# Kernel optimization log

Hardware: AMD Instinct MI355X
Metric: run time of the kernel (lower is better)

The kernel has to match this reference:

```python
import jax, jax.numpy as jnp
import numpy as np

EPS = 1e-5  # torch BatchNorm default eps, eval mode with running stats

def _bn(x, g, b, m, v):
    shp = (1, -1) + (1,) * (x.ndim - 2)
    return (x - m.reshape(shp)) * (g.reshape(shp) / jnp.sqrt(v.reshape(shp) + EPS)) + b.reshape(shp)

def _lrelu(x):
    return jnp.where(x > 0, x, 0.2 * x)

def setup_inputs() -> dict:
    key = jax.random.key(0)
    ks = jax.random.split(key, 20)
    B, N, K = 4, 2048, 32
    Cin, Cf, Co = 6, 64, 64  # in_channels, feat_channels, out_channels(==nhiddens)
    f32 = jnp.float32
    def randn(k, shape, s=1.0):
        return jax.random.normal(k, shape, f32) * s
    def bnp(k, c):
        k1, k2, k3, k4 = jax.random.split(k, 4)
        return (randn(k1, (c,)), randn(k2, (c,)), randn(k3, (c,), 0.1),
                jax.random.uniform(k4, (c,), f32, 0.5, 1.5))
    inp = {
        "x": randn(ks[0], (B, Cin, N, K)),          # knn_points
        "y": randn(ks[1], (B, Cf, N, K)),           # knn_feat
        "points": randn(ks[2], (B, Cin // 2, N)),
        "feat": randn(ks[3], (B, Cf // 2, N)),
        "Wq": randn(ks[4], (Cf, Cf // 2), 0.1),
        "Wpos1": randn(ks[5], (Cin, Cin // 2), 0.1),
        "Wpos2": randn(ks[6], (Cf, Cin), 0.1),
        "Wattn": randn(ks[7], (Co * Cin, Cf), 0.1),
        "Wlin": randn(ks[8], (Co, Co), 0.1),
        "Wres": randn(ks[9], (Co, Cf), 0.1),
    }
    for name, k, c in [("q", ks[10], Cf), ("p", ks[11], Cin), ("a", ks[12], Co * Cin),
                       ("1", ks[13], Co), ("l", ks[14], Co), ("r", ks[15], Co)]:
        g, b, m, v = bnp(k, c)
        inp["g" + name], inp["b" + name], inp["m" + name], inp["v" + name] = g, b, m, v
    return inp

def reference(x, y, points, feat, Wq, Wpos1, Wpos2, Wattn, Wlin, Wres,
              gq, bq, mq, vq, gp, bp, mp, vp, ga, ba, ma, va,
              g1, b1, m1, v1, gl, bl, ml, vl, gr, br, mr, vr):
    B, Cin, N, K = x.shape
    Cf = y.shape[1]
    Co = Wattn.shape[0] // Cin
    # query projection (conv1d 1x1 == per-point GEMM) + BN + LeakyReLU
    x_q = _lrelu(_bn(jnp.einsum('oi,bin->bon', Wq, feat), gq, bq, mq, vq))   # [B,Cf,N]
    # positional branch
    pos = _lrelu(_bn(jnp.einsum('oi,bin->bon', Wpos1, points), gp, bp, mp, vp))  # [B,Cin,N]
    pos = pos[:, :, :, None] - x                                             # [B,Cin,N,K]
    pos = jnp.einsum('oi,bink->bonk', Wpos2, pos)                            # [B,Cf,N,K]
    # vector (subtraction) attention, softmax over neighbors k
    attn = x_q[:, :, :, None] - y + pos                                      # [B,Cf,N,K]
    attn = jax.nn.softmax(attn / float(np.sqrt(Cf)), axis=-1)
    attn = _bn(jnp.einsum('oi,bink->bonk', Wattn, attn), ga, ba, ma, va)     # [B,Co*Cin,N,K]
    # per-point tiny matmul: [Co,Cin] @ [Cin] for every (b,n,k)
    attn = attn.transpose(0, 2, 3, 1).reshape(B, N, K, Co, Cin)
    out = jnp.einsum('bnkoi,bnki->bonk', attn, x.transpose(0, 2, 3, 1))      # [B,Co,N,K]
    h = _lrelu(_bn(out, g1, b1, m1, v1))
    h = _bn(jnp.einsum('oi,bink->bonk', Wlin, h), gl, bl, ml, vl)
    res = _bn(jnp.einsum('oi,bink->bonk', Wres, y), gr, br, mr, vr)
    return _lrelu(h + res)
```

## Files before the change

kernel.cpp:

```cpp
#include <hip/hip_runtime.h>

constexpr int NB  = 4;
constexpr int NPT = 2048;
constexpr int KNN = 32;
constexpr int CIN = 6;
constexpr int CF  = 64;
constexpr int CO  = 64;
constexpr float EPS = 1e-5f;

typedef short bf16x8 __attribute__((ext_vector_type(8)));
typedef float f32x4  __attribute__((ext_vector_type(4)));

constexpr size_t WS_WA  = 0;
constexpr size_t WS_WL  = 49152;
constexpr size_t WS_WR  = 57344;
constexpr size_t WS_BA  = 65536;
constexpr size_t WS_BNF = 67072;

__device__ __host__ inline unsigned short bf16_rne(float f) {
  unsigned u = __builtin_bit_cast(unsigned, f);
  u += 0x7fffu + ((u >> 16) & 1u);
  return (unsigned short)(u >> 16);
}

__global__ void setup_kernel(const float *Wattn, const float *Wlin, const float *Wres,
                             const float *ga, const float *ba, const float *ma, const float *va,
                             const float *g1, const float *b1, const float *m1, const float *v1,
                             const float *gl, const float *bl, const float *ml, const float *vl,
                             const float *gr, const float *br, const float *mr, const float *vr,
                             unsigned short *WAf, unsigned short *WLf, unsigned short *WRf,
                             float *baP, float *bnf) {
  const int t = blockIdx.x * blockDim.x + threadIdx.x;
  const int stride = gridDim.x * blockDim.x;
  for (int e = t; e < 6 * 4 * 2 * 64 * 8; e += stride) {
    const int j = e & 7, l = (e >> 3) & 63, ks = (e >> 9) & 1, ot = (e >> 10) & 3, i = e >> 12;
    const int m = l & 15, cg = l >> 4;
    const int cc = ks * 32 + cg * 8 + j;
    const int row = (ot * 16 + m) * CIN + i;
    const float sa = ga[row] * rsqrtf(va[row] + EPS);
    WAf[e] = bf16_rne(Wattn[row * CF + cc] * sa);
  }
  for (int e = t; e < 4 * 2 * 64 * 8; e += stride) {
    const int j = e & 7, l = (e >> 3) & 63, ks = (e >> 9) & 1, ot = e >> 10;
    const int m = l & 15;
    const int cc = ks * 32 + (l >> 4) * 8 + j;
    const int row = ot * 16 + m;
    const float sl = gl[row] * rsqrtf(vl[row] + EPS);
    const float sr = gr[row] * rsqrtf(vr[row] + EPS);
    WLf[e] = bf16_rne(Wlin[row * CF + cc] * sl);
    WRf[e] = bf16_rne(Wres[row * CF + cc] * sr);
  }
  for (int e = t; e < 384; e += stride) {
    const int i = e >> 6, o = e & 63;
    const int j0 = o * CIN + i;
    const float sa = ga[j0] * rsqrtf(va[j0] + EPS);
    baP[e] = ba[j0] - ma[j0] * sa;
  }
  for (int e = t; e < 64; e += stride) {
    const float s1v = g1[e] * rsqrtf(v1[e] + EPS);
    bnf[e]      = s1v;
    bnf[64 + e] = b1[e] - m1[e] * s1v;
    const float slv = gl[e] * rsqrtf(vl[e] + EPS);
    const float srv = gr[e] * rsqrtf(vr[e] + EPS);
    bnf[128 + e] = (bl[e] - ml[e] * slv) + (br[e] - mr[e] * srv);
  }
}

struct Params {
  const float *x, *y, *points, *feat;
  const float *Wq, *Wpos1, *Wpos2;
  const float *gq, *bq, *mq, *vq;
  const float *gp, *bp, *mp, *vp;
  const unsigned short *WAf, *WLf, *WRf;
  const float *baP, *bnf;
  float *out;
};

__global__ __launch_bounds__(256) void fused_pt_attn(Params p) {
  const int tid  = threadIdx.x;
  const int lane = tid & 63;
  const int wid  = tid >> 6;
  const int bid  = ((blockIdx.x & 7) << 8) + (blockIdx.x >> 3);
  const int pidx = bid * 4 + wid;
  const int b    = pidx >> 11;
  const int n    = pidx & (NPT - 1);

  __shared__ unsigned short s_B[4][2 * 2048];
  __shared__ float s_d[4][192];
  __shared__ float s_f[4][32];
  unsigned short *yB = s_B[wid];
  unsigned short *PB = s_B[wid] + 2048;
  float *dW = s_d[wid];
  float *fW = s_f[wid];

  float ftv = 0.f, ptv = 0.f;
  if (lane < 32) ftv = p.feat[((size_t)b * 32 + lane) * NPT + n];
  if (lane < 3)  ptv = p.points[((size_t)b * 3 + lane) * NPT + n];
  const int xi = lane >> 3, xk = (lane & 7) * 4;
  float4 x4 = make_float4(0.f, 0.f, 0.f, 0.f);
  if (lane < 48)
    x4 = *(const float4 *)(p.x + (((size_t)b * CIN + xi) * NPT + n) * KNN + xk);
  const float *w2p = p.Wpos2 + lane * 6;
  const float2 w2a = *(const float2 *)(w2p);
  const float2 w2b = *(const float2 *)(w2p + 2);
  const float2 w2c = *(const float2 *)(w2p + 4);
  const float w2[6] = {w2a.x, w2a.y, w2b.x, w2b.y, w2c.x, w2c.y};

  if (lane < 32) fW[lane] = ftv;

  const float pt0 = __shfl(ptv, 0), pt1 = __shfl(ptv, 1), pt2 = __shfl(ptv, 2);
  float pos1[6];
#pragma unroll
  for (int i = 0; i < 6; ++i) {
    const float a = p.Wpos1[i * 3 + 0] * pt0 + p.Wpos1[i * 3 + 1] * pt1 +
                    p.Wpos1[i * 3 + 2] * pt2;
    const float s = p.gp[i] * rsqrtf(p.vp[i] + EPS);
    const float v = fmaf(a, s, p.bp[i] - p.mp[i] * s);
    pos1[i] = v > 0.f ? v : 0.2f * v;
  }

  if (lane < 48) {
    float pi = pos1[0];
    pi = (xi == 1) ? pos1[1] : pi;
    pi = (xi == 2) ? pos1[2] : pi;
    pi = (xi == 3) ? pos1[3] : pi;
    pi = (xi == 4) ? pos1[4] : pi;
    pi = (xi == 5) ? pos1[5] : pi;
    *(float4 *)(dW + xi * 32 + xk) =
        make_float4(pi - x4.x, pi - x4.y, pi - x4.z, pi - x4.w);
  }

  float xq;
  {
    float acc = 0.f;
    const float *wq = p.Wq + lane * 32;
#pragma unroll
    for (int q = 0; q < 8; ++q) {
      const float4 w4 = *(const float4 *)(wq + q * 4);
      const float4 f4 = *(const float4 *)(fW + q * 4);
      acc = fmaf(w4.x, f4.x, fmaf(w4.y, f4.y, fmaf(w4.z, f4.z, fmaf(w4.w, f4.w, acc))));
    }
    const float s = p.gq[lane] * rsqrtf(p.vq[lane] + EPS);
    const float v = fmaf(acc, s, p.bq[lane] - p.mq[lane] * s);
    xq = v > 0.f ? v : 0.2f * v;
  }

  float pre[32];
#pragma unroll
  for (int k = 0; k < 32; ++k) pre[k] = 0.f;
#pragma unroll
  for (int i = 0; i < 6; ++i) {
    const float wv = w2[i];
#pragma unroll
    for (int q = 0; q < 8; ++q) {
      const float4 d4 = *(const float4 *)(dW + i * 32 + q * 4);
      pre[q * 4 + 0] = fmaf(wv, d4.x, pre[q * 4 + 0]);
      pre[q * 4 + 1] = fmaf(wv, d4.y, pre[q * 4 + 1]);
      pre[q * 4 + 2] = fmaf(wv, d4.z, pre[q * 4 + 2]);
      pre[q * 4 + 3] = fmaf(wv, d4.w, pre[q * 4 + 3]);
    }
  }

  const float *yrow = p.y + (((size_t)b * CF + lane) * NPT + n) * KNN;
#pragma unroll
  for (int q = 0; q < 8; ++q) {
    const float4 y4 = *(const float4 *)(yrow + q * 4);
    const float yv[4] = {y4.x, y4.y, y4.z, y4.w};
#pragma unroll
    for (int j = 0; j < 4; ++j) {
      const int k = q * 4 + j;
      yB[k * 64 + (lane ^ ((k & 7) << 3))] = bf16_rne(yv[j]);
      pre[k] = (xq - yv[j] + pre[k]) * 0.125f;
    }
  }

  float mx = pre[0];
#pragma unroll
  for (int k = 1; k < 32; ++k) mx = fmaxf(mx, pre[k]);
  float sum = 0.f;
#pragma unroll
  for (int k = 0; k < 32; ++k) { pre[k] = __expf(pre[k] - mx); sum += pre[k]; }
  const float inv = 1.f / sum;
#pragma unroll
  for (int k = 0; k < 32; ++k)
    PB[k * 64 + (lane ^ ((k & 7) << 3))] = bf16_rne(pre[k] * inv);

  const int og = lane >> 4, kl = lane & 15;

  float xvv[6][2];
#pragma unroll
  for (int i = 0; i < 6; ++i)
#pragma unroll
    for (int nt = 0; nt < 2; ++nt)
      xvv[i][nt] = pos1[i] - dW[i * 32 + kl + nt * 16];

  bf16x8 Ba[2][2];
#pragma unroll
  for (int ks = 0; ks < 2; ++ks)
#pragma unroll
    for (int nt = 0; nt < 2; ++nt) {
      const int kcol = kl + nt * 16;
      Ba[ks][nt] = *(const bf16x8 *)(PB + kcol * 64 + ((ks * 32 + og * 8) ^ ((kcol & 7) << 3)));
    }

  const bf16x8 *WAv = (const bf16x8 *)p.WAf;
#pragma unroll
  for (int ot = 0; ot < 4; ++ot) {
    float out1[2][4] = {{0.f, 0.f, 0.f, 0.f}, {0.f, 0.f, 0.f, 0.f}};
#pragma unroll
    for (int i = 0; i < 6; ++i) {
      const bf16x8 A0 = WAv[((i * 4 + ot) * 2 + 0) * 64 + lane];
      const bf16x8 A1 = WAv[((i * 4 + ot) * 2 + 1) * 64 + lane];
      const f32x4 ba4 = *(const f32x4 *)(p.baP + i * 64 + ot * 16 + og * 4);
#pragma unroll
      for (int nt = 0; nt < 2; ++nt) {
        f32x4 g = {0.f, 0.f, 0.f, 0.f};
        g = __builtin_amdgcn_mfma_f32_16x16x32_bf16(A0, Ba[0][nt], g, 0, 0, 0);
        g = __builtin_amdgcn_mfma_f32_16x16x32_bf16(A1, Ba[1][nt], g, 0, 0, 0);
        const float xv = xvv[i][nt];
#pragma unroll
        for (int r = 0; r < 4; ++r)
          out1[nt][r] = fmaf(g[r] + ba4[r], xv, out1[nt][r]);
      }
    }
    const f32x4 s14 = *(const f32x4 *)(p.bnf + 0 * 64 + ot * 16 + og * 4);
    const f32x4 b14 = *(const f32x4 *)(p.bnf + 1 * 64 + ot * 16 + og * 4);
#pragma unroll
    for (int nt = 0; nt < 2; ++nt) {
      const int kcol = kl + nt * 16;
      unsigned hp[4];
#pragma unroll
      for (int r = 0; r < 4; ++r) {
        const float t = fmaf(s14[r], out1[nt][r], b14[r]);
        hp[r] = bf16_rne(t > 0.f ? t : 0.2f * t);
      }
      const int idx = kcol * 64 + ((ot * 16 + og * 4) ^ ((kcol & 7) << 3));
      *(uint2 *)(PB + idx) = make_uint2(hp[0] | (hp[1] << 16), hp[2] | (hp[3] << 16));
    }
  }

  bf16x8 Bh[2][2], By[2][2];
#pragma unroll
  for (int ks = 0; ks < 2; ++ks)
#pragma unroll
    for (int nt = 0; nt < 2; ++nt) {
      const int kcol = kl + nt * 16;
      const int off = kcol * 64 + ((ks * 32 + og * 8) ^ ((kcol & 7) << 3));
      Bh[ks][nt] = *(const bf16x8 *)(PB + off);
      By[ks][nt] = *(const bf16x8 *)(yB + off);
    }
  const bf16x8 *WLv = (const bf16x8 *)p.WLf;
  const bf16x8 *WRv = (const bf16x8 *)p.WRf;
#pragma unroll
  for (int ot = 0; ot < 4; ++ot) {
    const bf16x8 L0 = WLv[(ot * 2 + 0) * 64 + lane];
    const bf16x8 L1 = WLv[(ot * 2 + 1) * 64 + lane];
    const bf16x8 R0 = WRv[(ot * 2 + 0) * 64 + lane];
    const bf16x8 R1 = WRv[(ot * 2 + 1) * 64 + lane];
    const f32x4 blr = *(const f32x4 *)(p.bnf + 2 * 64 + ot * 16 + og * 4);
#pragma unroll
    for (int nt = 0; nt < 2; ++nt) {
      f32x4 a = {0.f, 0.f, 0.f, 0.f};
      a = __builtin_amdgcn_mfma_f32_16x16x32_bf16(L0, Bh[0][nt], a, 0, 0, 0);
      a = __builtin_amdgcn_mfma_f32_16x16x32_bf16(L1, Bh[1][nt], a, 0, 0, 0);
      a = __builtin_amdgcn_mfma_f32_16x16x32_bf16(R0, By[0][nt], a, 0, 0, 0);
      a = __builtin_amdgcn_mfma_f32_16x16x32_bf16(R1, By[1][nt], a, 0, 0, 0);
      const int kcol = kl + nt * 16;
      float *ob = p.out + (((size_t)(b * CO + ot * 16 + og * 4)) * NPT + n) * KNN + kcol;
#pragma unroll
      for (int r = 0; r < 4; ++r) {
        const float v = a[r] + blr[r];
        ob[(size_t)r * NPT * KNN] = v > 0.f ? v : 0.2f * v;
      }
    }
  }
}

extern "C" void kernel_launch(void *const *d_in, const int *in_sizes, int n_in,
                              void *d_out, int out_size, void *d_ws, size_t ws_size,
                              hipStream_t stream) {
  char *ws = (char *)d_ws;
  unsigned short *WAf = (unsigned short *)(ws + WS_WA);
  unsigned short *WLf = (unsigned short *)(ws + WS_WL);
  unsigned short *WRf = (unsigned short *)(ws + WS_WR);
  float *baP = (float *)(ws + WS_BA);
  float *bnf = (float *)(ws + WS_BNF);

  setup_kernel<<<dim3(96), dim3(256), 0, stream>>>(
      (const float *)d_in[7], (const float *)d_in[8], (const float *)d_in[9],
      (const float *)d_in[18], (const float *)d_in[19], (const float *)d_in[20], (const float *)d_in[21],
      (const float *)d_in[22], (const float *)d_in[23], (const float *)d_in[24], (const float *)d_in[25],
      (const float *)d_in[26], (const float *)d_in[27], (const float *)d_in[28], (const float *)d_in[29],
      (const float *)d_in[30], (const float *)d_in[31], (const float *)d_in[32], (const float *)d_in[33],
      WAf, WLf, WRf, baP, bnf);

  Params p;
  p.x      = (const float *)d_in[0];
  p.y      = (const float *)d_in[1];
  p.points = (const float *)d_in[2];
  p.feat   = (const float *)d_in[3];
  p.Wq     = (const float *)d_in[4];
  p.Wpos1  = (const float *)d_in[5];
  p.Wpos2  = (const float *)d_in[6];
  p.gq = (const float *)d_in[10]; p.bq = (const float *)d_in[11];
  p.mq = (const float *)d_in[12]; p.vq = (const float *)d_in[13];
  p.gp = (const float *)d_in[14]; p.bp = (const float *)d_in[15];
  p.mp = (const float *)d_in[16]; p.vp = (const float *)d_in[17];
  p.WAf = WAf; p.WLf = WLf; p.WRf = WRf;
  p.baP = baP; p.bnf = bnf;
  p.out = (float *)d_out;

  fused_pt_attn<<<dim3(NB * NPT / 4), dim3(256), 0, stream>>>(p);
}
```

Before: 66.88 us.

## Split output-channel tiles across waves sharing point pairs to reuse weight fragments

Each wave used to process one point through all four output-channel tiles. Now pairs of waves share two points through shared memory, and each wave handles half the output tiles for both points. Each weight fragment loaded from global memory is therefore reused for two points, halving per-wave weight traffic. The positional-term algebra is also refactored so pos1·W2 folds into a per-lane scalar alpha. In exchange the kernel adds three block-wide barriers and keeps more live registers for two points' fragments.

After: 76.30 us. +14.1%, slower.

```diff
diff --git a/kernel.cpp b/kernel.cpp
--- a/kernel.cpp
+++ b/kernel.cpp
@@ -81,178 +81,203 @@
   const int lane = tid & 63;
   const int wid  = tid >> 6;
   const int bid  = ((blockIdx.x & 7) << 8) + (blockIdx.x >> 3);
-  const int pidx = bid * 4 + wid;
-  const int b    = pidx >> 11;
-  const int n    = pidx & (NPT - 1);
-
-  __shared__ unsigned short s_B[4][2 * 2048];
-  __shared__ float s_d[4][192];
+  const int b    = bid >> 9;
+  const int n    = (bid * 4 + wid) & (NPT - 1);
+
+  __shared__ unsigned short s_Y[4][2048];
+  __shared__ unsigned short s_P[4][2048];
+  __shared__ float s_x[4][192];
   __shared__ float s_f[4][32];
-  unsigned short *yB = s_B[wid];
-  unsigned short *PB = s_B[wid] + 2048;
-  float *dW = s_d[wid];
+  unsigned short *YB = s_Y[wid];
+  unsigned short *PB = s_P[wid];
+  float *xW = s_x[wid];
   float *fW = s_f[wid];
 
-  float ftv = 0.f, ptv = 0.f;
-  if (lane < 32) ftv = p.feat[((size_t)b * 32 + lane) * NPT + n];
-  if (lane < 3)  ptv = p.points[((size_t)b * 3 + lane) * NPT + n];
-  const int xi = lane >> 3, xk = (lane & 7) * 4;
-  float4 x4 = make_float4(0.f, 0.f, 0.f, 0.f);
-  if (lane < 48)
-    x4 = *(const float4 *)(p.x + (((size_t)b * CIN + xi) * NPT + n) * KNN + xk);
-  const float *w2p = p.Wpos2 + lane * 6;
-  const float2 w2a = *(const float2 *)(w2p);
-  const float2 w2b = *(const float2 *)(w2p + 2);
-  const float2 w2c = *(const float2 *)(w2p + 4);
-  const float w2[6] = {w2a.x, w2a.y, w2b.x, w2b.y, w2c.x, w2c.y};
-
-  if (lane < 32) fW[lane] = ftv;
-
-  const float pt0 = __shfl(ptv, 0), pt1 = __shfl(ptv, 1), pt2 = __shfl(ptv, 2);
-  float pos1[6];
-#pragma unroll
-  for (int i = 0; i < 6; ++i) {
-    const float a = p.Wpos1[i * 3 + 0] * pt0 + p.Wpos1[i * 3 + 1] * pt1 +
-                    p.Wpos1[i * 3 + 2] * pt2;
-    const float s = p.gp[i] * rsqrtf(p.vp[i] + EPS);
-    const float v = fmaf(a, s, p.bp[i] - p.mp[i] * s);
-    pos1[i] = v > 0.f ? v : 0.2f * v;
-  }
-
-  if (lane < 48) {
-    float pi = pos1[0];
-    pi = (xi == 1) ? pos1[1] : pi;
-    pi = (xi == 2) ? pos1[2] : pi;
-    pi = (xi == 3) ? pos1[3] : pi;
-    pi = (xi == 4) ? pos1[4] : pi;
-    pi = (xi == 5) ? pos1[5] : pi;
-    *(float4 *)(dW + xi * 32 + xk) =
-        make_float4(pi - x4.x, pi - x4.y, pi - x4.z, pi - x4.w);
-  }
-
-  float xq;
   {
-    float acc = 0.f;
-    const float *wq = p.Wq + lane * 32;
+    float ftv = 0.f, ptv = 0.f;
+    if (lane < 32) ftv = p.feat[((size_t)b * 32 + lane) * NPT + n];
+    if (lane < 3)  ptv = p.points[((size_t)b * 3 + lane) * NPT + n];
+    const int xi = lane >> 3, xk = (lane & 7) * 4;
+    float4 x4 = make_float4(0.f, 0.f, 0.f, 0.f);
+    if (lane < 48)
+      x4 = *(const float4 *)(p.x + (((size_t)b * CIN + xi) * NPT + n) * KNN + xk);
+    const float *w2p = p.Wpos2 + lane * 6;
+    const float2 w2a = *(const float2 *)(w2p);
+    const float2 w2b = *(const float2 *)(w2p + 2);
+    const float2 w2c = *(const float2 *)(w2p + 4);
+    const float w2[6] = {w2a.x, w2a.y, w2b.x, w2b.y, w2c.x, w2c.y};
+
+    if (lane < 32) fW[lane] = ftv;
+    if (lane < 48) *(float4 *)(xW + xi * 32 + xk) = x4;
+
+    const float pt0 = __shfl(ptv, 0), pt1 = __shfl(ptv, 1), pt2 = __shfl(ptv, 2);
+    float pos1[6];
+#pragma unroll
+    for (int i = 0; i < 6; ++i) {
+      const float a = p.Wpos1[i * 3 + 0] * pt0 + p.Wpos1[i * 3 + 1] * pt1 +
+                      p.Wpos1[i * 3 + 2] * pt2;
+      const float s = p.gp[i] * rsqrtf(p.vp[i] + EPS);
+      const float v = fmaf(a, s, p.bp[i] - p.mp[i] * s);
+      pos1[i] = v > 0.f ? v : 0.2f * v;
+    }
+
+    float xq;
+    {
+      float acc = 0.f;
+      const float *wq = p.Wq + lane * 32;
+#pragma unroll
+      for (int q = 0; q < 8; ++q) {
+        const float4 w4 = *(const float4 *)(wq + q * 4);
+        const float4 f4 = *(const float4 *)(fW + q * 4);
+        acc = fmaf(w4.x, f4.x, fmaf(w4.y, f4.y, fmaf(w4.z, f4.z, fmaf(w4.w, f4.w, acc))));
+      }
+      const float s = p.gq[lane] * rsqrtf(p.vq[lane] + EPS);
+      const float v = fmaf(acc, s, p.bq[lane] - p.mq[lane] * s);
+      xq = v > 0.f ? v : 0.2f * v;
+    }
+
+    float alpha = xq;
+#pragma unroll
+    for (int i = 0; i < 6; ++i) alpha = fmaf(w2[i], pos1[i], alpha);
+
+    float pre[32];
+#pragma unroll
+    for (int k = 0; k < 32; ++k) pre[k] = 0.f;
+#pragma unroll
+    for (int i = 0; i < 6; ++i) {
+      const float wv = w2[i];
+#pragma unroll
+      for (int q = 0; q < 8; ++q) {
+        const float4 d4 = *(const float4 *)(xW + i * 32 + q * 4);
+        pre[q * 4 + 0] = fmaf(wv, d4.x, pre[q * 4 + 0]);
+        pre[q * 4 + 1] = fmaf(wv, d4.y, pre[q * 4 + 1]);
+        pre[q * 4 + 2] = fmaf(wv, d4.z, pre[q * 4 + 2]);
+        pre[q * 4 + 3] = fmaf(wv, d4.w, pre[q * 4 + 3]);
+      }
+    }
+
+    const float *yrow = p.y + (((size_t)b * CF + lane) * NPT + n) * KNN;
 #pragma unroll
     for (int q = 0; q < 8; ++q) {
-      const float4 w4 = *(const float4 *)(wq + q * 4);
-      const float4 f4 = *(const float4 *)(fW + q * 4);
-      acc = fmaf(w4.x, f4.x, fmaf(w4.y, f4.y, fmaf(w4.z, f4.z, fmaf(w4.w, f4.w, acc))));
-    }
-    const float s = p.gq[lane] * rsqrtf(p.vq[lane] + EPS);
-    const float v = fmaf(acc, s, p.bq[lane] - p.mq[lane] * s);
-    xq = v > 0.f ? v : 0.2f * v;
-  }
-
-  float pre[32];
-#pragma unroll
-  for (int k = 0; k < 32; ++k) pre[k] = 0.f;
-#pragma unroll
-  for (int i = 0; i < 6; ++i) {
-    const float wv = w2[i];
-#pragma unroll
-    for (int q = 0; q < 8; ++q) {
-      const float4 d4 = *(const float4 *)(dW + i * 32 + q * 4);
-      pre[q * 4 + 0] = fmaf(wv, d4.x, pre[q * 4 + 0]);
-      pre[q * 4 + 1] = fmaf(wv, d4.y, pre[q * 4 + 1]);
-      pre[q * 4 + 2] = fmaf(wv, d4.z, pre[q * 4 + 2]);
-      pre[q * 4 + 3] = fmaf(wv, d4.w, pre[q * 4 + 3]);
-    }
-  }
-
-  const float *yrow = p.y + (((size_t)b * CF + lane) * NPT + n) * KNN;
-#pragma unroll
-  for (int q = 0; q < 8; ++q) {
-    const float4 y4 = *(const float4 *)(yrow + q * 4);
-    const float yv[4] = {y4.x, y4.y, y4.z, y4.w};
-#pragma unroll
-    for (int j = 0; j < 4; ++j) {
-      const int k = q * 4 + j;
-      yB[k * 64 + (lane ^ ((k & 7) << 3))] = bf16_rne(yv[j]);
-      pre[k] = (xq - yv[j] + pre[k]) * 0.125f;
-    }
-  }
-
-  float mx = pre[0];
-#pragma unroll
-  for (int k = 1; k < 32; ++k) mx = fmaxf(mx, pre[k]);
-  float sum = 0.f;
-#pragma unroll
-  for (int k = 0; k < 32; ++k) { pre[k] = __expf(pre[k] - mx); sum += pre[k]; }
-  const float inv = 1.f / sum;
-#pragma unroll
-  for (int k = 0; k < 32; ++k)
-    PB[k * 64 + (lane ^ ((k & 7) << 3))] = bf16_rne(pre[k] * inv);
-
+      const float4 y4 = *(const float4 *)(yrow + q * 4);
+      const float yv[4] = {y4.x, y4.y, y4.z, y4.w};
+#pragma unroll
+      for (int j = 0; j < 4; ++j) {
+        const int k = q * 4 + j;
+        YB[k * 64 + (lane ^ ((k & 7) << 3))] = bf16_rne(yv[j]);
+        pre[k] = (alpha - pre[k] - yv[j]) * 0.125f;
+      }
+    }
+
+    float mx = pre[0];
+#pragma unroll
+    for (int k = 1; k < 32; ++k) mx = fmaxf(mx, pre[k]);
+    float sum = 0.f;
+#pragma unroll
+    for (int k = 0; k < 32; ++k) { pre[k] = __expf(pre[k] - mx); sum += pre[k]; }
+    const float inv = 1.f / sum;
+#pragma unroll
+    for (int k = 0; k < 32; ++k)
+      PB[k * 64 + (lane ^ ((k & 7) << 3))] = bf16_rne(pre[k] * inv);
+  }
+  __syncthreads();
+
+  const int s0  = wid & 2;
+  const int s1  = s0 + 1;
+  const int otb = (wid & 1) * 2;
+  const int n0  = (bid * 4 + s0) & (NPT - 1);
   const int og = lane >> 4, kl = lane & 15;
-
-  float xvv[6][2];
+  const int swz = (kl & 7) << 3;
+
+  bf16x8 Ba0[2][2], Ba1[2][2];
+#pragma unroll
+  for (int ks = 0; ks < 2; ++ks)
+#pragma unroll
+    for (int nt = 0; nt < 2; ++nt) {
+      const int off = (kl + nt * 16) * 64 + ((ks * 32 + og * 8) ^ swz);
+      Ba0[ks][nt] = *(const bf16x8 *)(s_P[s0] + off);
+      Ba1[ks][nt] = *(const bf16x8 *)(s_P[s1] + off);
+    }
+  float xv0[6][2], xv1[6][2];
 #pragma unroll
   for (int i = 0; i < 6; ++i)
 #pragma unroll
-    for (int nt = 0; nt < 2; ++nt)
-      xvv[i][nt] = pos1[i] - dW[i * 32 + kl + nt * 16];
-
-  bf16x8 Ba[2][2];
-#pragma unroll
-  for (int ks = 0; ks < 2; ++ks)
-#pragma unroll
-    for (int nt = 0; nt < 2; ++nt) {
-      const int kcol = kl + nt * 16;
-      Ba[ks][nt] = *(const bf16x8 *)(PB + kcol * 64 + ((ks * 32 + og * 8) ^ ((kcol & 7) << 3)));
-    }
+    for (int nt = 0; nt < 2; ++nt) {
+      xv0[i][nt] = s_x[s0][i * 32 + kl + nt * 16];
+      xv1[i][nt] = s_x[s1][i * 32 + kl + nt * 16];
+    }
+  __syncthreads();
 
   const bf16x8 *WAv = (const bf16x8 *)p.WAf;
 #pragma unroll
-  for (int ot = 0; ot < 4; ++ot) {
-    float out1[2][4] = {{0.f, 0.f, 0.f, 0.f}, {0.f, 0.f, 0.f, 0.f}};
+  for (int ot2 = 0; ot2 < 2; ++ot2) {
+    const int ot = otb + ot2;
+    f32x4 o00 = {0.f, 0.f, 0.f, 0.f}, o01 = o00, o10 = o00, o11 = o00;
 #pragma unroll
     for (int i = 0; i < 6; ++i) {
       const bf16x8 A0 = WAv[((i * 4 + ot) * 2 + 0) * 64 + lane];
       const bf16x8 A1 = WAv[((i * 4 + ot) * 2 + 1) * 64 + lane];
       const f32x4 ba4 = *(const f32x4 *)(p.baP + i * 64 + ot * 16 + og * 4);
-#pragma unroll
-      for (int nt = 0; nt < 2; ++nt) {
-        f32x4 g = {0.f, 0.f, 0.f, 0.f};
-        g = __builtin_amdgcn_mfma_f32_16x16x32_bf16(A0, Ba[0][nt], g, 0, 0, 0);
-        g = __builtin_amdgcn_mfma_f32_16x16x32_bf16(A1, Ba[1][nt], g, 0, 0, 0);
-        const float xv = xvv[i][nt];
-#pragma unroll
-        for (int r = 0; r < 4; ++r)
-          out1[nt][r] = fmaf(g[r] + ba4[r], xv, out1[nt][r]);
-      }
+      f32x4 g;
+      g = (f32x4){0.f, 0.f, 0.f, 0.f};
+      g = __builtin_amdgcn_mfma_f32_16x16x32_bf16(A0, Ba0[0][0], g, 0, 0, 0);
+      g = __builtin_amdgcn_mfma_f32_16x16x32_bf16(A1, Ba0[1][0], g, 0, 0, 0);
+#pragma unroll
+      for (int r = 0; r < 4; ++r) o00[r] = fmaf(g[r] + ba4[r], xv0[i][0], o00[r]);
+      g = (f32x4){0.f, 0.f, 0.f, 0.f};
+      g = __builtin_amdgcn_mfma_f32_16x16x32_bf16(A0, Ba0[0][1], g, 0, 0, 0);
+      g = __builtin_amdgcn_mfma_f32_16x16x32_bf16(A1, Ba0[1][1], g, 0, 0, 0);
+#pragma unroll
+      for (int r = 0; r < 4; ++r) o01[r] = fmaf(g[r] + ba4[r], xv0[i][1], o01[r]);
+      g = (f32x4){0.f, 0.f, 0.f, 0.f};
+      g = __builtin_amdgcn_mfma_f32_16x16x32_bf16(A0, Ba1[0][0], g, 0, 0, 0);
+      g = __builtin_amdgcn_mfma_f32_16x16x32_bf16(A1, Ba1[1][0], g, 0, 0, 0);
+#pragma unroll
+      for (int r = 0; r < 4; ++r) o10[r] = fmaf(g[r] + ba4[r], xv1[i][0], o10[r]);
+      g = (f32x4){0.f, 0.f, 0.f, 0.f};
+      g = __builtin_amdgcn_mfma_f32_16x16x32_bf16(A0, Ba1[0][1], g, 0, 0, 0);
+      g = __builtin_amdgcn_mfma_f32_16x16x32_bf16(A1, Ba1[1][1], g, 0, 0, 0);
+#pragma unroll
+      for (int r = 0; r < 4; ++r) o11[r] = fmaf(g[r] + ba4[r], xv1[i][1], o11[r]);
     }
     const f32x4 s14 = *(const f32x4 *)(p.bnf + 0 * 64 + ot * 16 + og * 4);
     const f32x4 b14 = *(const f32x4 *)(p.bnf + 1 * 64 + ot * 16 + og * 4);
 #pragma unroll
     for (int nt = 0; nt < 2; ++nt) {
-      const int kcol = kl + nt * 16;
-      unsigned hp[4];
+      const int idx = (kl + nt * 16) * 64 + ((ot * 16 + og * 4) ^ swz);
+      const f32x4 &q0 = nt ? o01 : o00;
+      const f32x4 &q1 = nt ? o11 : o10;
+      unsigned h0[4], h1[4];
 #pragma unroll
       for (int r = 0; r < 4; ++r) {
-        const float t = fmaf(s14[r], out1[nt][r], b14[r]);
-        hp[r] = bf16_rne(t > 0.f ? t : 0.2f * t);
-      }
-      const int idx = kcol * 64 + ((ot * 16 + og * 4) ^ ((kcol & 7) << 3));
-      *(uint2 *)(PB + idx) = make_uint2(hp[0] | (hp[1] << 16), hp[2] | (hp[3] << 16));
-    }
-  }
-
-  bf16x8 Bh[2][2], By[2][2];
+        const float t0 = fmaf(s14[r], q0[r], b14[r]);
+        const float t1 = fmaf(s14[r], q1[r], b14[r]);
+        h0[r] = bf16_rne(t0 > 0.f ? t0 : 0.2f * t0);
+        h1[r] = bf16_rne(t1 > 0.f ? t1 : 0.2f * t1);
+      }
+      *(uint2 *)(s_P[s0] + idx) = make_uint2(h0[0] | (h0[1] << 16), h0[2] | (h0[3] << 16));
+      *(uint2 *)(s_P[s1] + idx) = make_uint2(h1[0] | (h1[1] << 16), h1[2] | (h1[3] << 16));
+    }
+  }
+  __syncthreads();
+
+  bf16x8 Bh0[2][2], Bh1[2][2], By0[2][2], By1[2][2];
 #pragma unroll
   for (int ks = 0; ks < 2; ++ks)
 #pragma unroll
     for (int nt = 0; nt < 2; ++nt) {
-      const int kcol = kl + nt * 16;
-      const int off = kcol * 64 + ((ks * 32 + og * 8) ^ ((kcol & 7) << 3));
-      Bh[ks][nt] = *(const bf16x8 *)(PB + off);
-      By[ks][nt] = *(const bf16x8 *)(yB + off);
-    }
+      const int off = (kl + nt * 16) * 64 + ((ks * 32 + og * 8) ^ swz);
+      Bh0[ks][nt] = *(const bf16x8 *)(s_P[s0] + off);
+      Bh1[ks][nt] = *(const bf16x8 *)(s_P[s1] + off);
+      By0[ks][nt] = *(const bf16x8 *)(s_Y[s0] + off);
+      By1[ks][nt] = *(const bf16x8 *)(s_Y[s1] + off);
+    }
+
   const bf16x8 *WLv = (const bf16x8 *)p.WLf;
   const bf16x8 *WRv = (const bf16x8 *)p.WRf;
 #pragma unroll
-  for (int ot = 0; ot < 4; ++ot) {
+  for (int ot2 = 0; ot2 < 2; ++ot2) {
+    const int ot = otb + ot2;
     const bf16x8 L0 = WLv[(ot * 2 + 0) * 64 + lane];
     const bf16x8 L1 = WLv[(ot * 2 + 1) * 64 + lane];
     const bf16x8 R0 = WRv[(ot * 2 + 0) * 64 + lane];
@@ -260,17 +285,23 @@
     const f32x4 blr = *(const f32x4 *)(p.bnf + 2 * 64 + ot * 16 + og * 4);
 #pragma unroll
     for (int nt = 0; nt < 2; ++nt) {
-      f32x4 a = {0.f, 0.f, 0.f, 0.f};
-      a = __builtin_amdgcn_mfma_f32_16x16x32_bf16(L0, Bh[0][nt], a, 0, 0, 0);
-      a = __builtin_amdgcn_mfma_f32_16x16x32_bf16(L1, Bh[1][nt], a, 0, 0, 0);
-      a = __builtin_amdgcn_mfma_f32_16x16x32_bf16(R0, By[0][nt], a, 0, 0, 0);
-      a = __builtin_amdgcn_mfma_f32_16x16x32_bf16(R1, By[1][nt], a, 0, 0, 0);
+      f32x4 a0 = {0.f, 0.f, 0.f, 0.f}, a1 = a0;
+      a0 = __builtin_amdgcn_mfma_f32_16x16x32_bf16(L0, Bh0[0][nt], a0, 0, 0, 0);
+      a0 = __builtin_amdgcn_mfma_f32_16x16x32_bf16(L1, Bh0[1][nt], a0, 0, 0, 0);
+      a0 = __builtin_amdgcn_mfma_f32_16x16x32_bf16(R0, By0[0][nt], a0, 0, 0, 0);
+      a0 = __builtin_amdgcn_mfma_f32_16x16x32_bf16(R1, By0[1][nt], a0, 0, 0, 0);
+      a1 = __builtin_amdgcn_mfma_f32_16x16x32_bf16(L0, Bh1[0][nt], a1, 0, 0, 0);
+      a1 = __builtin_amdgcn_mfma_f32_16x16x32_bf16(L1, Bh1[1][nt], a1, 0, 0, 0);
+      a1 = __builtin_amdgcn_mfma_f32_16x16x32_bf16(R0, By1[0][nt], a1, 0, 0, 0);
+      a1 = __builtin_amdgcn_mfma_f32_16x16x32_bf16(R1, By1[1][nt], a1, 0, 0, 0);
       const int kcol = kl + nt * 16;
-      float *ob = p.out + (((size_t)(b * CO + ot * 16 + og * 4)) * NPT + n) * KNN + kcol;
+      float *ob = p.out + (((size_t)(b * CO + ot * 16 + og * 4)) * NPT + n0) * KNN + kcol;
 #pragma unroll
       for (int r = 0; r < 4; ++r) {
-        const float v = a[r] + blr[r];
-        ob[(size_t)r * NPT * KNN] = v > 0.f ? v : 0.2f * v;
+        const float v0 = a0[r] + blr[r];
+        const float v1 = a1[r] + blr[r];
+        ob[(size_t)r * NPT * KNN]       = v0 > 0.f ? v0 : 0.2f * v0;
+        ob[(size_t)r * NPT * KNN + KNN] = v1 > 0.f ? v1 : 0.2f * v1;
       }
     }
   }
```
